# Optimization experiments

Measured on AMD Instinct MI355X. Metric: run time of the kernel, lower is better.

Reference implementation:

```python
import jax, jax.numpy as jnp
import numpy as np
from jax import lax

B, H, W, C = 8, 64, 64, 256
OUT = 1024          # channels (final conv filters)
KS = 3              # kernel_size
GROUP_DIV = 1
N_GROUPS = C // GROUP_DIV  # 256 -> depthwise-style grouped convs
DN = ('NHWC', 'HWIO', 'NHWC')
EPS = 1e-5


def setup_inputs() -> dict:
    key = jax.random.key(0)
    ks = jax.random.split(key, 6)
    x = jax.random.normal(ks[0], (B, H, W, C), jnp.float32)
    w_spatial = jax.random.normal(ks[1], (B, KS, KS, C // N_GROUPS, C), jnp.float32) * 0.05
    w_pointwise = jax.random.normal(ks[2], (B, 1, 1, C // N_GROUPS, C), jnp.float32) * 0.05
    bias = jax.random.normal(ks[3], (B, C), jnp.float32) * 0.05
    conv_w = jax.random.normal(ks[4], (KS, KS, C, OUT), jnp.float32) * (1.0 / np.sqrt(KS * KS * C))
    conv_b = jnp.zeros((OUT,), jnp.float32)
    return {"x": x, "w_spatial": w_spatial, "w_pointwise": w_pointwise,
            "bias": bias, "conv_w": conv_w, "conv_b": conv_b}


def _instance_norm(x):
    # TF: (x - mean) / (std + eps), population std over H,W per sample/channel
    mean = jnp.mean(x, axis=(1, 2), keepdims=True)
    std = jnp.sqrt(jnp.mean((x - mean) ** 2, axis=(1, 2), keepdims=True))
    return (x - mean) / (std + EPS)


def _per_sample(xi, ws, wp, b):
    # xi: [H,W,C]; ws: [ks,ks,1,C]; wp: [1,1,1,C]; b: [C]
    y = lax.conv_general_dilated(xi[None], ws, (1, 1), 'SAME',
                                 dimension_numbers=DN,
                                 feature_group_count=N_GROUPS)
    y = lax.conv_general_dilated(y, wp, (1, 1), 'VALID',
                                 dimension_numbers=DN,
                                 feature_group_count=N_GROUPS) + b
    return y[0]


def reference(x, w_spatial, w_pointwise, bias, conv_w, conv_b):
    x = _instance_norm(x)
    # batched per-sample dynamic grouped spatial + pointwise conv
    x = jax.vmap(_per_sample)(x, w_spatial, w_pointwise, bias)  # [B,H,W,C]
    # shared 3x3 SAME conv C -> OUT with bias
    y = lax.conv_general_dilated(x, conv_w, (1, 1), 'SAME',
                                 dimension_numbers=DN) + conv_b
    return y
```

## Files before the change

kernel.cpp:

```cpp
#include <hip/hip_runtime.h>
#include <hip/hip_bf16.h>
#include <cstdint>
#include <cstddef>

constexpr int Bn   = 8;
constexpr int Hn   = 64;
constexpr int Wn   = 64;
constexpr int Cn   = 256;
constexpr int OUTC = 1024;
constexpr int HPAD = 66;
constexpr int WPAD = 66;
#define EPS 1e-5f

typedef __attribute__((ext_vector_type(4))) float f32x4;
typedef __bf16 bf16x8 __attribute__((ext_vector_type(8)));

__device__ __forceinline__ void gload_lds16(const void* g, void* l) {
    __builtin_amdgcn_global_load_lds(
        (__attribute__((address_space(1))) void*)g,
        (__attribute__((address_space(3))) void*)l,
        16, 0, 0);
}

__global__ __launch_bounds__(256) void k0_transpose_w(const float* __restrict__ conv_w,
                                                      __hip_bfloat16* __restrict__ wT) {
    __shared__ float tile[64][65];
    const int tap = blockIdx.x;
    const int ct  = blockIdx.y;
    const int ot  = blockIdx.z;
    const int t   = threadIdx.x;
    const int lo  = t & 63;
    const int cq  = t >> 6;

#pragma unroll
    for (int k = 0; k < 16; ++k) {
        int ci = k * 4 + cq;
        tile[lo][ci] = conv_w[((size_t)(tap * Cn + ct * 64 + ci)) * OUTC + ot * 64 + lo];
    }
    __syncthreads();
#pragma unroll
    for (int k = 0; k < 16; ++k) {
        int oo = k * 4 + cq;
        wT[((size_t)(tap * OUTC + ot * 64 + oo)) * Cn + ct * 64 + lo] =
            __float2bfloat16(tile[oo][lo]);
    }
}

__global__ __launch_bounds__(1024) void k1_stats_partial(const float* __restrict__ x,
                                                         float* __restrict__ ps,
                                                         float* __restrict__ pq) {
    __shared__ float sb[2][4][256];
    const int bh = blockIdx.x;
    const int tid = threadIdx.x;
    const int c = tid & 255;
    const int s = tid >> 8;
    const float* row = x + (size_t)bh * Wn * Cn + (size_t)s * 16 * Cn + c;
    float sm = 0.f, q = 0.f;
#pragma unroll
    for (int w = 0; w < 16; ++w) {
        float v = row[(size_t)w * Cn];
        sm += v; q += v * v;
    }
    sb[0][s][c] = sm; sb[1][s][c] = q;
    __syncthreads();
    if (s == 0) {
        float S = 0.f, Q = 0.f;
#pragma unroll
        for (int k = 0; k < 4; ++k) { S += sb[0][k][c]; Q += sb[1][k][c]; }
        ps[bh * Cn + c] = S;
        pq[bh * Cn + c] = Q;
    }
}

__global__ __launch_bounds__(1024) void k2_stats_final(const float* __restrict__ ps,
                                                       const float* __restrict__ pq,
                                                       float* __restrict__ scale,
                                                       float* __restrict__ shift) {
    __shared__ float sb[2][4][256];
    const int b = blockIdx.x;
    const int tid = threadIdx.x;
    const int c = tid & 255;
    const int qd = tid >> 8;
    float S = 0.f, Q = 0.f;
#pragma unroll 4
    for (int i = 0; i < 16; ++i) {
        int h = qd * 16 + i;
        S += ps[(b * Hn + h) * Cn + c];
        Q += pq[(b * Hn + h) * Cn + c];
    }
    sb[0][qd][c] = S; sb[1][qd][c] = Q;
    __syncthreads();
    if (qd == 0) {
        float s2 = 0.f, q2 = 0.f;
#pragma unroll
        for (int k = 0; k < 4; ++k) { s2 += sb[0][k][c]; q2 += sb[1][k][c]; }
        const float inv = 1.f / (float)(Hn * Wn);
        float mean = s2 * inv;
        float var  = fmaxf(q2 * inv - mean * mean, 0.f);
        float sc   = 1.f / (sqrtf(var) + EPS);
        scale[b * Cn + c] = sc;
        shift[b * Cn + c] = -mean * sc;
    }
}

__global__ __launch_bounds__(256) void k3_dwconv(const float* __restrict__ x,
                                                 const float* __restrict__ w_sp,
                                                 const float* __restrict__ w_pw,
                                                 const float* __restrict__ bias,
                                                 const float* __restrict__ scale,
                                                 const float* __restrict__ shift,
                                                 __hip_bfloat16* __restrict__ tpad) {
    const int bq = blockIdx.x;
    const int wq = bq & 3;
    const int bh = bq >> 2;
    const int b  = bh / HPAD;
    const int hp = bh - b * HPAD;
    const int c  = threadIdx.x;
    __hip_bfloat16* orow = tpad + ((size_t)(b * HPAD + hp)) * WPAD * Cn + c;
    const __hip_bfloat16 z = __float2bfloat16(0.f);

    if (hp == 0 || hp == HPAD - 1) {
        int wlo = wq * 17, whi = wlo + 17 < WPAD ? wlo + 17 : WPAD;
        for (int wp = wlo; wp < whi; ++wp) orow[(size_t)wp * Cn] = z;
        return;
    }
    const int h = hp - 1;
    const float sc = scale[b * Cn + c];
    const float sh = shift[b * Cn + c];
    float w9[9];
#pragma unroll
    for (int k = 0; k < 9; ++k) w9[k] = w_sp[(b * 9 + k) * Cn + c];
    const float pw = w_pw[b * Cn + c];
    const float bv = bias[b * Cn + c];
    const float* xb = x + (size_t)b * Hn * Wn * Cn + c;

    bool rv[3];
#pragma unroll
    for (int r = 0; r < 3; ++r) { int rr = h - 1 + r; rv[r] = (rr >= 0 && rr < Hn); }

    if (wq == 0) orow[0] = z;
    if (wq == 3) orow[(size_t)(WPAD - 1) * Cn] = z;

    const int w0 = wq * 16;
    float win[3][3];
#pragma unroll
    for (int r = 0; r < 3; ++r) {
        win[r][0] = (rv[r] && w0 > 0)
                    ? (xb[((size_t)(h - 1 + r) * Wn + (w0 - 1)) * Cn] * sc + sh) : 0.f;
        win[r][1] = rv[r] ? (xb[((size_t)(h - 1 + r) * Wn + w0) * Cn] * sc + sh) : 0.f;
    }
    for (int i = 0; i < 16; ++i) {
        const int w = w0 + i;
#pragma unroll
        for (int r = 0; r < 3; ++r)
            win[r][2] = (rv[r] && (w + 1) < Wn)
                        ? (xb[((size_t)(h - 1 + r) * Wn + (w + 1)) * Cn] * sc + sh) : 0.f;
        float y = 0.f;
#pragma unroll
        for (int r = 0; r < 3; ++r)
#pragma unroll
            for (int qq = 0; qq < 3; ++qq)
                y += win[r][qq] * w9[r * 3 + qq];
        orow[(size_t)(w + 1) * Cn] = __float2bfloat16(y * pw + bv);
#pragma unroll
        for (int r = 0; r < 3; ++r) { win[r][0] = win[r][1]; win[r][1] = win[r][2]; }
    }
}

constexpr int KSTEPS = 72;
constexpr int BUFSZ  = 32768;

__global__ __launch_bounds__(512, 2) void k4_gemm(const __hip_bfloat16* __restrict__ tpad,
                                                  const __hip_bfloat16* __restrict__ wT,
                                                  const float* __restrict__ conv_b,
                                                  float* __restrict__ out) {
    __shared__ __align__(16) char smem[4 * BUFSZ];

    const int tid  = threadIdx.x;
    const int lane = tid & 63;
    const int wv   = tid >> 6;
    const int wm   = wv >> 2;
    const int wn   = wv & 3;
    const int g    = lane >> 4, l15 = lane & 15;

    const int bid = blockIdx.x;
    const int mt  = (bid & 7) * 16 + ((bid >> 3) & 15);
    const int nt  = bid >> 7;
    const int pixbase = mt * 256;
    const int b       = mt >> 4;
    const int hbase   = (mt & 15) * 4;
    const int obase   = nt * 256;

    int aoff[2], boff[2];
#pragma unroll
    for (int j = 0; j < 2; ++j) {
        int u = j * 512 + tid;
        int r = u >> 3, p = u & 7;
        int l = p ^ (r & 7);
        int pix = 2 * r + (l >> 2);
        int hh  = hbase + (pix >> 6);
        int ww  = pix & 63;
        aoff[j] = ((b * HPAD + hh) * WPAD + ww) * Cn + (l & 3) * 8;
        boff[j] = (obase + 2 * r + (l >> 2)) * Cn + (l & 3) * 8;
    }

    auto stageS = [&](int s) {
        const int tap = s >> 3, ks = s & 7;
        const int kh  = tap / 3, kw = tap - 3 * kh;
        const __hip_bfloat16* aS = tpad + ((kh * WPAD + kw) * Cn + ks * 32);
        const __hip_bfloat16* bS = wT + (size_t)tap * (OUTC * Cn) + ks * 32;
        char* buf = smem + (s & 3) * BUFSZ;
        gload_lds16(aS + aoff[0], buf + (size_t)(0 * 512 + wv * 64) * 16);
        gload_lds16(aS + aoff[1], buf + (size_t)(1 * 512 + wv * 64) * 16);
        gload_lds16(bS + boff[0], buf + 16384 + (size_t)(0 * 512 + wv * 64) * 16);
        gload_lds16(bS + boff[1], buf + 16384 + (size_t)(1 * 512 + wv * 64) * 16);
    };

    f32x4 acc[8][4] = {};

    auto substep = [&](int t, bool dostage, int spre) {
        char* Ab = smem + (t & 3) * BUFSZ;
        char* Bb = Ab + 16384;
        bf16x8 bfr[4], af[8];
#pragma unroll
        for (int n = 0; n < 4; ++n) {
            int o = wn * 64 + n * 16 + l15;
            int r = o >> 1;
            bfr[n] = *(const bf16x8*)(Bb + r * 128 +
                         ((((o & 1) << 2) | g) ^ (r & 7)) * 16);
        }
#pragma unroll
        for (int m = 0; m < 8; ++m) {
            int pix = wm * 128 + m * 16 + l15;
            int r = pix >> 1;
            af[m] = *(const bf16x8*)(Ab + r * 128 +
                         ((((pix & 1) << 2) | g) ^ (r & 7)) * 16);
        }
        if (dostage) stageS(spre);
        __builtin_amdgcn_s_setprio(1);
#pragma unroll
        for (int m = 0; m < 8; ++m)
#pragma unroll
            for (int n = 0; n < 4; ++n)
                acc[m][n] = __builtin_amdgcn_mfma_f32_16x16x32_bf16(
                    af[m], bfr[n], acc[m][n], 0, 0, 0);
        __builtin_amdgcn_s_setprio(0);
    };

    stageS(0);
    stageS(1);
    asm volatile("s_waitcnt vmcnt(0)" ::: "memory");
    __builtin_amdgcn_s_barrier();
    __builtin_amdgcn_sched_barrier(0);

#pragma unroll 1
    for (int body = 0; body < KSTEPS / 2; ++body) {
        const int t0 = 2 * body;
        substep(t0,     t0 + 2 < KSTEPS, t0 + 2);
        substep(t0 + 1, t0 + 3 < KSTEPS, t0 + 3);
        __builtin_amdgcn_sched_barrier(0);
        if (body + 1 < KSTEPS / 2) {
            asm volatile("s_waitcnt vmcnt(0)" ::: "memory");
            __builtin_amdgcn_s_barrier();
            __builtin_amdgcn_sched_barrier(0);
        }
    }

    float cb[4];
#pragma unroll
    for (int n = 0; n < 4; ++n) cb[n] = conv_b[obase + wn * 64 + n * 16 + l15];
#pragma unroll
    for (int m = 0; m < 8; ++m) {
#pragma unroll
        for (int j = 0; j < 4; ++j) {
            int r = pixbase + wm * 128 + m * 16 + g * 4 + j;
            float* orow = out + (size_t)r * OUTC + obase + wn * 64 + l15;
#pragma unroll
            for (int n = 0; n < 4; ++n)
                orow[n * 16] = acc[m][n][j] + cb[n];
        }
    }
}

extern "C" void kernel_launch(void* const* d_in, const int* in_sizes, int n_in,
                              void* d_out, int out_size, void* d_ws, size_t ws_size,
                              hipStream_t stream) {
    const float* x      = (const float*)d_in[0];
    const float* w_sp   = (const float*)d_in[1];
    const float* w_pw   = (const float*)d_in[2];
    const float* bias   = (const float*)d_in[3];
    const float* conv_w = (const float*)d_in[4];
    const float* conv_b = (const float*)d_in[5];
    float* out = (float*)d_out;

    char* ws = (char*)d_ws;
    __hip_bfloat16* wT    = (__hip_bfloat16*)(ws);
    float*          ps    = (float*)(ws + 4718592);
    float*          pq    = (float*)(ws + 4718592 + 524288);
    float*          scale = (float*)(ws + 5767168);
    float*          shift = (float*)(ws + 5775360);
    __hip_bfloat16* tpad  = (__hip_bfloat16*)(ws + 5783552);

    k0_transpose_w<<<dim3(9, 4, 16), 256, 0, stream>>>(conv_w, wT);
    k1_stats_partial<<<Bn * Hn, 1024, 0, stream>>>(x, ps, pq);
    k2_stats_final<<<Bn, 1024, 0, stream>>>(ps, pq, scale, shift);
    k3_dwconv<<<Bn * HPAD * 4, 256, 0, stream>>>(x, w_sp, w_pw, bias, scale, shift, tpad);
    k4_gemm<<<512, 512, 0, stream>>>(tpad, wT, conv_b, out);
}
```

Measured before the change: 170.9 us.

## Shrink GEMM tile to 128x256 and load B fragments directly into registers

The implicit-GEMM conv kernel moves from 256x256 tiles with 8 waves to 128x256 tiles with 4 waves and doubles the grid. Weight (B) fragments are no longer staged through LDS; each wave reads its own B slice from global memory into registers, double-buffered one step ahead. Only activations (A) go through LDS, so the LDS footprint per block drops to a quarter. A-fragment reads are interleaved with MFMAs, the block-to-tile mapping is changed to group by XCD, and the wait before each barrier is relaxed to vmcnt(4). The cost is less reuse of each staged tile and uncoalesced per-lane global B loads that depend on the cache.

```diff
diff --git a/kernel.cpp b/kernel.cpp
--- a/kernel.cpp
+++ b/kernel.cpp
@@ -168,9 +168,9 @@
 }
 
 constexpr int KSTEPS = 72;
-constexpr int BUFSZ  = 32768;
-
-__global__ __launch_bounds__(512, 2) void k4_gemm(const __hip_bfloat16* __restrict__ tpad,
+constexpr int BUFSZ  = 8192;
+
+__global__ __launch_bounds__(256, 2) void k4_gemm(const __hip_bfloat16* __restrict__ tpad,
                                                   const __hip_bfloat16* __restrict__ wT,
                                                   const float* __restrict__ conv_b,
                                                   float* __restrict__ out) {
@@ -179,88 +179,98 @@
     const int tid  = threadIdx.x;
     const int lane = tid & 63;
     const int wv   = tid >> 6;
-    const int wm   = wv >> 2;
-    const int wn   = wv & 3;
+    const int wn   = wv;
     const int g    = lane >> 4, l15 = lane & 15;
 
     const int bid = blockIdx.x;
-    const int mt  = (bid & 7) * 16 + ((bid >> 3) & 15);
-    const int nt  = bid >> 7;
-    const int pixbase = mt * 256;
-    const int b       = mt >> 4;
-    const int hbase   = (mt & 15) * 4;
+    const int xcd = bid & 7;
+    const int idx = bid >> 3;
+    const int nt  = xcd & 3;
+    const int mt  = (xcd >> 2) * 128 + idx;
+    const int pixbase = mt * 128;
+    const int b       = mt >> 5;
+    const int hbase   = (mt & 31) * 2;
     const int obase   = nt * 256;
 
-    int aoff[2], boff[2];
+    int aoff[2];
 #pragma unroll
     for (int j = 0; j < 2; ++j) {
-        int u = j * 512 + tid;
+        int u = j * 256 + tid;
         int r = u >> 3, p = u & 7;
         int l = p ^ (r & 7);
         int pix = 2 * r + (l >> 2);
         int hh  = hbase + (pix >> 6);
         int ww  = pix & 63;
         aoff[j] = ((b * HPAD + hh) * WPAD + ww) * Cn + (l & 3) * 8;
-        boff[j] = (obase + 2 * r + (l >> 2)) * Cn + (l & 3) * 8;
     }
 
     auto stageS = [&](int s) {
         const int tap = s >> 3, ks = s & 7;
         const int kh  = tap / 3, kw = tap - 3 * kh;
         const __hip_bfloat16* aS = tpad + ((kh * WPAD + kw) * Cn + ks * 32);
-        const __hip_bfloat16* bS = wT + (size_t)tap * (OUTC * Cn) + ks * 32;
         char* buf = smem + (s & 3) * BUFSZ;
-        gload_lds16(aS + aoff[0], buf + (size_t)(0 * 512 + wv * 64) * 16);
-        gload_lds16(aS + aoff[1], buf + (size_t)(1 * 512 + wv * 64) * 16);
-        gload_lds16(bS + boff[0], buf + 16384 + (size_t)(0 * 512 + wv * 64) * 16);
-        gload_lds16(bS + boff[1], buf + 16384 + (size_t)(1 * 512 + wv * 64) * 16);
+        gload_lds16(aS + aoff[0], buf + (size_t)(0 * 256 + wv * 64) * 16);
+        gload_lds16(aS + aoff[1], buf + (size_t)(1 * 256 + wv * 64) * 16);
     };
 
+    const __hip_bfloat16* bRow = wT + (size_t)(obase + wn * 64 + l15) * Cn + g * 8;
+    auto loadB = [&](int s, bf16x8 (&dst)[4]) {
+        const int tap = s >> 3, ks = s & 7;
+        const __hip_bfloat16* p0 = bRow + (size_t)tap * (OUTC * Cn) + ks * 32;
+#pragma unroll
+        for (int n = 0; n < 4; ++n)
+            dst[n] = *(const bf16x8*)(p0 + (size_t)n * 16 * Cn);
+    };
+
     f32x4 acc[8][4] = {};
 
-    auto substep = [&](int t, bool dostage, int spre) {
+    auto substep = [&](int t, bf16x8 (&bcur)[4], bf16x8 (&bnxt)[4]) {
         char* Ab = smem + (t & 3) * BUFSZ;
-        char* Bb = Ab + 16384;
-        bf16x8 bfr[4], af[8];
-#pragma unroll
-        for (int n = 0; n < 4; ++n) {
-            int o = wn * 64 + n * 16 + l15;
-            int r = o >> 1;
-            bfr[n] = *(const bf16x8*)(Bb + r * 128 +
-                         ((((o & 1) << 2) | g) ^ (r & 7)) * 16);
+        if (t + 2 < KSTEPS) stageS(t + 2);
+        if (t + 1 < KSTEPS) loadB(t + 1, bnxt);
+
+        auto rdA = [&](int m) -> bf16x8 {
+            int r = m * 8 + (l15 >> 1);
+            int slot = ((((l15 & 1) << 2) | g) ^ (r & 7));
+            return *(const bf16x8*)(Ab + r * 128 + slot * 16);
+        };
+#define MF(a_, m_)                                                            \
+        {                                                                     \
+            _Pragma("unroll")                                                 \
+            for (int n = 0; n < 4; ++n)                                       \
+                acc[m_][n] = __builtin_amdgcn_mfma_f32_16x16x32_bf16(         \
+                    a_, bcur[n], acc[m_][n], 0, 0, 0);                        \
         }
-#pragma unroll
-        for (int m = 0; m < 8; ++m) {
-            int pix = wm * 128 + m * 16 + l15;
-            int r = pix >> 1;
-            af[m] = *(const bf16x8*)(Ab + r * 128 +
-                         ((((pix & 1) << 2) | g) ^ (r & 7)) * 16);
-        }
-        if (dostage) stageS(spre);
+        bf16x8 a0 = rdA(0), a1 = rdA(1);
+        bf16x8 a2 = rdA(2), a3 = rdA(3);
         __builtin_amdgcn_s_setprio(1);
-#pragma unroll
-        for (int m = 0; m < 8; ++m)
-#pragma unroll
-            for (int n = 0; n < 4; ++n)
-                acc[m][n] = __builtin_amdgcn_mfma_f32_16x16x32_bf16(
-                    af[m], bfr[n], acc[m][n], 0, 0, 0);
+        MF(a0, 0); MF(a1, 1);
+        bf16x8 a4 = rdA(4), a5 = rdA(5);
+        MF(a2, 2); MF(a3, 3);
+        bf16x8 a6 = rdA(6), a7 = rdA(7);
+        MF(a4, 4); MF(a5, 5);
+        MF(a6, 6); MF(a7, 7);
         __builtin_amdgcn_s_setprio(0);
+#undef MF
     };
+
+    bf16x8 bA[4], bB[4];
 
     stageS(0);
     stageS(1);
-    asm volatile("s_waitcnt vmcnt(0)" ::: "memory");
+    loadB(0, bA);
+    asm volatile("s_waitcnt vmcnt(4)" ::: "memory");
     __builtin_amdgcn_s_barrier();
     __builtin_amdgcn_sched_barrier(0);
 
 #pragma unroll 1
     for (int body = 0; body < KSTEPS / 2; ++body) {
         const int t0 = 2 * body;
-        substep(t0,     t0 + 2 < KSTEPS, t0 + 2);
-        substep(t0 + 1, t0 + 3 < KSTEPS, t0 + 3);
+        substep(t0,     bA, bB);
+        substep(t0 + 1, bB, bA);
         __builtin_amdgcn_sched_barrier(0);
         if (body + 1 < KSTEPS / 2) {
-            asm volatile("s_waitcnt vmcnt(0)" ::: "memory");
+            asm volatile("s_waitcnt vmcnt(4)" ::: "memory");
             __builtin_amdgcn_s_barrier();
             __builtin_amdgcn_sched_barrier(0);
         }
@@ -273,7 +283,7 @@
     for (int m = 0; m < 8; ++m) {
 #pragma unroll
         for (int j = 0; j < 4; ++j) {
-            int r = pixbase + wm * 128 + m * 16 + g * 4 + j;
+            int r = pixbase + m * 16 + g * 4 + j;
             float* orow = out + (size_t)r * OUTC + obase + wn * 64 + l15;
 #pragma unroll
             for (int n = 0; n < 4; ++n)
@@ -305,5 +315,5 @@
     k1_stats_partial<<<Bn * Hn, 1024, 0, stream>>>(x, ps, pq);
     k2_stats_final<<<Bn, 1024, 0, stream>>>(ps, pq, scale, shift);
     k3_dwconv<<<Bn * HPAD * 4, 256, 0, stream>>>(x, w_sp, w_pw, bias, scale, shift, tpad);
-    k4_gemm<<<512, 512, 0, stream>>>(tpad, wT, conv_b, out);
-}
+    k4_gemm<<<1024, 256, 0, stream>>>(tpad, wT, conv_b, out);
+}
```

After: 243.8 us. 42.7% more time.

## Stagger LDS reads across wave halves and precompute swizzled LDS offsets

Applied to the files above, without the earlier changes.

The GEMM main loop now precomputes the swizzled LDS read offsets once, so each fragment read is a base plus a constant. The loop also splits waves by wm. Waves with wm==0 read and compute each substep in turn. The other waves prefetch both substeps' A fragments before the first MFMA cluster, so LDS reads and MFMA bursts fall at different times in the two halves. The aim is to cut LDS bank contention and address arithmetic and get better MFMA/LDS overlap, at the cost of more VGPRs in the prefetching branch and possible occupancy or spill risk.

```diff
diff --git a/kernel.cpp b/kernel.cpp
--- a/kernel.cpp
+++ b/kernel.cpp
@@ -216,36 +216,32 @@
         gload_lds16(bS + boff[1], buf + 16384 + (size_t)(1 * 512 + wv * 64) * 16);
     };
 
+    const int slot = ((((l15 & 1) << 2) | g) ^ ((l15 >> 1) & 7)) * 16;
+    const int aRd  = wm * 8192 + (l15 >> 1) * 128 + slot;
+    const int bRd  = 16384 + wn * 4096 + (l15 >> 1) * 128 + slot;
+
     f32x4 acc[8][4] = {};
 
-    auto substep = [&](int t, bool dostage, int spre) {
-        char* Ab = smem + (t & 3) * BUFSZ;
-        char* Bb = Ab + 16384;
-        bf16x8 bfr[4], af[8];
-#pragma unroll
-        for (int n = 0; n < 4; ++n) {
-            int o = wn * 64 + n * 16 + l15;
-            int r = o >> 1;
-            bfr[n] = *(const bf16x8*)(Bb + r * 128 +
-                         ((((o & 1) << 2) | g) ^ (r & 7)) * 16);
-        }
-#pragma unroll
-        for (int m = 0; m < 8; ++m) {
-            int pix = wm * 128 + m * 16 + l15;
-            int r = pix >> 1;
-            af[m] = *(const bf16x8*)(Ab + r * 128 +
-                         ((((pix & 1) << 2) | g) ^ (r & 7)) * 16);
-        }
-        if (dostage) stageS(spre);
-        __builtin_amdgcn_s_setprio(1);
-#pragma unroll
-        for (int m = 0; m < 8; ++m)
-#pragma unroll
-            for (int n = 0; n < 4; ++n)
-                acc[m][n] = __builtin_amdgcn_mfma_f32_16x16x32_bf16(
-                    af[m], bfr[n], acc[m][n], 0, 0, 0);
-        __builtin_amdgcn_s_setprio(0);
+    auto readA = [&](char* cb, bf16x8 (&af)[8]) {
+#pragma unroll
+        for (int m = 0; m < 8; ++m) af[m] = *(const bf16x8*)(cb + aRd + m * 1024);
     };
+    auto readB = [&](char* cb, bf16x8 (&bf)[4]) {
+#pragma unroll
+        for (int n = 0; n < 4; ++n) bf[n] = *(const bf16x8*)(cb + bRd + n * 1024);
+    };
+
+#define MFMA_CLUSTER(af_, bf_)                                                \
+    {                                                                         \
+        __builtin_amdgcn_s_setprio(1);                                        \
+        _Pragma("unroll")                                                     \
+        for (int m = 0; m < 8; ++m)                                           \
+            _Pragma("unroll")                                                 \
+            for (int n = 0; n < 4; ++n)                                       \
+                acc[m][n] = __builtin_amdgcn_mfma_f32_16x16x32_bf16(          \
+                    af_[m], bf_[n], acc[m][n], 0, 0, 0);                      \
+        __builtin_amdgcn_s_setprio(0);                                        \
+    }
 
     stageS(0);
     stageS(1);
@@ -256,8 +252,36 @@
 #pragma unroll 1
     for (int body = 0; body < KSTEPS / 2; ++body) {
         const int t0 = 2 * body;
-        substep(t0,     t0 + 2 < KSTEPS, t0 + 2);
-        substep(t0 + 1, t0 + 3 < KSTEPS, t0 + 3);
+        char* c0 = smem + (t0 & 3) * BUFSZ;
+        char* c1 = smem + ((t0 + 1) & 3) * BUFSZ;
+        const bool st2 = (t0 + 2 < KSTEPS);
+        const bool st3 = (t0 + 3 < KSTEPS);
+
+        if (wm == 0) {
+            bf16x8 af[8], bfr[4];
+            readB(c0, bfr); readA(c0, af);
+            if (st2) stageS(t0 + 2);
+            __builtin_amdgcn_sched_barrier(0);
+            MFMA_CLUSTER(af, bfr);
+            __builtin_amdgcn_sched_barrier(0);
+            readB(c1, bfr); readA(c1, af);
+            if (st3) stageS(t0 + 3);
+            __builtin_amdgcn_sched_barrier(0);
+            MFMA_CLUSTER(af, bfr);
+        } else {
+            bf16x8 af0[8], bf0[4], af1[8], bf1[4];
+            readB(c0, bf0); readA(c0, af0);
+            if (st2) stageS(t0 + 2);
+            readA(c1, af1);
+            if (st3) stageS(t0 + 3);
+            __builtin_amdgcn_sched_barrier(0);
+            MFMA_CLUSTER(af0, bf0);
+            __builtin_amdgcn_sched_barrier(0);
+            readB(c1, bf1);
+            __builtin_amdgcn_sched_barrier(0);
+            MFMA_CLUSTER(af1, bf1);
+        }
+
         __builtin_amdgcn_sched_barrier(0);
         if (body + 1 < KSTEPS / 2) {
             asm volatile("s_waitcnt vmcnt(0)" ::: "memory");
@@ -265,10 +289,11 @@
             __builtin_amdgcn_sched_barrier(0);
         }
     }
-
-    float cb[4];
-#pragma unroll
-    for (int n = 0; n < 4; ++n) cb[n] = conv_b[obase + wn * 64 + n * 16 + l15];
+#undef MFMA_CLUSTER
+
+    float cb2[4];
+#pragma unroll
+    for (int n = 0; n < 4; ++n) cb2[n] = conv_b[obase + wn * 64 + n * 16 + l15];
 #pragma unroll
     for (int m = 0; m < 8; ++m) {
 #pragma unroll
@@ -277,7 +302,7 @@
             float* orow = out + (size_t)r * OUTC + obase + wn * 64 + l15;
 #pragma unroll
             for (int n = 0; n < 4; ++n)
-                orow[n * 16] = acc[m][n][j] + cb[n];
+                orow[n * 16] = acc[m][n][j] + cb2[n];
         }
     }
 }
```

Result: no change. 168.8 us (median of 2 runs) (-1.2%).
